# Performance work log

Hardware: AMD Instinct MI355X
Metric: run time of the kernel (lower is better)

Reference implementation:

```python
import jax, jax.numpy as jnp
import numpy as np

D_MODEL = 1024
D_FF = 4096
NUM_EXPERTS = 8
TOP_K = 2  # expert_capacity


def setup_inputs() -> dict:
    key = jax.random.key(0)
    ks = jax.random.split(key, 7)
    s_in = 1.0 / np.sqrt(D_MODEL)
    s_ff = 1.0 / np.sqrt(D_FF)
    x = jax.random.normal(ks[0], (2, 2048, D_MODEL), dtype=jnp.float32)
    gate_w = jax.random.uniform(ks[1], (NUM_EXPERTS, D_MODEL), jnp.float32, -s_in, s_in)
    gate_b = jax.random.uniform(ks[2], (NUM_EXPERTS,), jnp.float32, -s_in, s_in)
    w1 = jax.random.uniform(ks[3], (NUM_EXPERTS, D_MODEL, D_FF), jnp.float32, -s_in, s_in)
    b1 = jax.random.uniform(ks[4], (NUM_EXPERTS, D_FF), jnp.float32, -s_in, s_in)
    w2 = jax.random.uniform(ks[5], (NUM_EXPERTS, D_FF, D_MODEL), jnp.float32, -s_ff, s_ff)
    b2 = jax.random.uniform(ks[6], (NUM_EXPERTS, D_MODEL), jnp.float32, -s_ff, s_ff)
    return {"x": x, "gate_w": gate_w, "gate_b": gate_b,
            "w1": w1, "b1": b1, "w2": w2, "b2": b2}


def reference(x, gate_w, gate_b, w1, b1, w2, b2):
    E = gate_w.shape[0]
    # Router
    logits = jnp.einsum('bsd,ed->bse', x, gate_w) + gate_b  # [B,S,E]
    top_vals, top_idx = jax.lax.top_k(logits, TOP_K)        # [B,S,K]
    top_w = jax.nn.softmax(top_vals, axis=-1)               # softmax over the top-k logits
    probs = jax.nn.softmax(logits, axis=-1)
    usage = probs.mean(axis=(0, 1))                         # [E]
    load_balancing_loss = E * jnp.sum(usage ** 2) - 1.0
    # Combine weights: sum over top-k slots of weight * one_hot(expert)
    combine = jnp.sum(top_w[..., None] * jax.nn.one_hot(top_idx, E, dtype=x.dtype), axis=2)  # [B,S,E]
    # All experts over all tokens (faithful to the naive dense-then-mask module)
    h = jax.nn.gelu(jnp.einsum('bsd,edf->ebsf', x, w1) + b1[:, None, None, :], approximate=False)
    expert_out = jnp.einsum('ebsf,efd->ebsd', h, w2) + b2[:, None, None, :]  # [E,B,S,D]
    output = jnp.einsum('bse,ebsd->bsd', combine, expert_out)
    return output, load_balancing_loss
```

## Files before the change

kernel.cpp:

```cpp
#include <hip/hip_runtime.h>
#include <hip/hip_bf16.h>
#include <math.h>


#define D_MODEL 1024
#define D_FF    4096
#define NE      8
#define NTOK    4096
#define CAP     4096

typedef __attribute__((ext_vector_type(4))) float f32x4;
typedef __attribute__((ext_vector_type(8))) short s16x8;

__device__ __forceinline__ short f2bf(float f) {
    union { float f; unsigned u; } v; v.f = f;
    unsigned r = v.u + 0x7FFFu + ((v.u >> 16) & 1u);
    return (short)(r >> 16);
}

__device__ __forceinline__ void gload16(const void* g, void* l) {
    __builtin_amdgcn_global_load_lds(
        (const __attribute__((address_space(1))) unsigned*)g,
        (__attribute__((address_space(3))) unsigned*)l, 16, 0, 0);
}

__global__ __launch_bounds__(256) void router_kernel(
    const float* __restrict__ x, const float* __restrict__ gw,
    const float* __restrict__ gb,
    float* __restrict__ usage, int* __restrict__ eidx, float* __restrict__ wgt)
{
    __shared__ float s_gw[NE][D_MODEL];
    __shared__ float s_usage[NE];
    int tid = threadIdx.x;
    for (int i = tid * 4; i < NE * D_MODEL; i += 256 * 4)
        *(f32x4*)&s_gw[0][i] = *(const f32x4*)(gw + i);
    if (tid < NE) s_usage[tid] = 0.f;
    __syncthreads();

    int wid = tid >> 6, lane = tid & 63;
    int wave_stride = gridDim.x * 4;
    float l_usage[NE];
#pragma unroll
    for (int e = 0; e < NE; e++) l_usage[e] = 0.f;

    for (int t = blockIdx.x * 4 + wid; t < NTOK; t += wave_stride) {
        const float* xr = x + (size_t)t * D_MODEL;
        float acc[NE];
#pragma unroll
        for (int e = 0; e < NE; e++) acc[e] = 0.f;
        for (int i = lane * 4; i < D_MODEL; i += 64 * 4) {
            f32x4 xv = *(const f32x4*)(xr + i);
#pragma unroll
            for (int e = 0; e < NE; e++) {
                f32x4 gv = *(const f32x4*)&s_gw[e][i];
                acc[e] += xv[0]*gv[0] + xv[1]*gv[1] + xv[2]*gv[2] + xv[3]*gv[3];
            }
        }
#pragma unroll
        for (int e = 0; e < NE; e++) {
            float a = acc[e];
            for (int off = 32; off; off >>= 1) a += __shfl_down(a, off);
            acc[e] = a;
        }
        if (lane == 0) {
            float logits[NE];
            float mx = -1e30f;
#pragma unroll
            for (int e = 0; e < NE; e++) { logits[e] = acc[e] + gb[e]; mx = fmaxf(mx, logits[e]); }
            float se = 0.f;
            float pe[NE];
#pragma unroll
            for (int e = 0; e < NE; e++) { pe[e] = expf(logits[e] - mx); se += pe[e]; }
            float inv = 1.f / se;
#pragma unroll
            for (int e = 0; e < NE; e++) l_usage[e] += pe[e] * inv;
            int i0 = 0;
#pragma unroll
            for (int e = 1; e < NE; e++) if (logits[e] > logits[i0]) i0 = e;
            int i1 = -1;
#pragma unroll
            for (int e = 0; e < NE; e++) {
                if (e == i0) continue;
                if (i1 < 0 || logits[e] > logits[i1]) i1 = e;
            }
            float w0 = 1.f / (1.f + expf(logits[i1] - logits[i0]));
            eidx[t] = i0 | (i1 << 8);
            wgt[t] = w0;
        }
    }
    if (lane == 0) {
#pragma unroll
        for (int e = 0; e < NE; e++) atomicAdd(&s_usage[e], l_usage[e]);
    }
    __syncthreads();
    if (tid < NE) atomicAdd(&usage[tid], s_usage[tid]);
}

__global__ __launch_bounds__(256) void build_lists(
    const int* __restrict__ eidx, const float* __restrict__ wgt,
    int* __restrict__ cnt, int* __restrict__ tok_list, float* __restrict__ wt_list)
{
    int e = blockIdx.x;
    __shared__ int s_cnt;
    if (threadIdx.x == 0) s_cnt = 0;
    __syncthreads();
    for (int t = threadIdx.x; t < NTOK; t += 256) {
        int p = eidx[t];
        float w0 = wgt[t];
        if ((p & 255) == e) {
            int s = atomicAdd(&s_cnt, 1);
            tok_list[e * CAP + s] = t; wt_list[e * CAP + s] = w0;
        }
        if ((p >> 8) == e) {
            int s = atomicAdd(&s_cnt, 1);
            tok_list[e * CAP + s] = t; wt_list[e * CAP + s] = 1.f - w0;
        }
    }
    __syncthreads();
    if (threadIdx.x == 0) cnt[e] = s_cnt;
}

__global__ void compute_offsets(const int* __restrict__ cnt, int* __restrict__ offsets)
{
    int o = 0;
    for (int e = 0; e < NE; e++) { offsets[e] = o; o += cnt[e]; }
}

__global__ void write_loss(const float* __restrict__ usage, float* __restrict__ out_loss)
{
    float s = 0.f;
    for (int e = 0; e < NE; e++) { float u = usage[e] / (float)NTOK; s += u * u; }
    *out_loss = (float)NE * s - 1.f;
}

__global__ __launch_bounds__(256) void cvt_x_kernel(
    const float* __restrict__ x, short* __restrict__ xb)
{
    int i = (blockIdx.x * 256 + threadIdx.x) * 8;
    f32x4 a = *(const f32x4*)(x + i);
    f32x4 b = *(const f32x4*)(x + i + 4);
    s16x8 r;
    r[0]=f2bf(a[0]); r[1]=f2bf(a[1]); r[2]=f2bf(a[2]); r[3]=f2bf(a[3]);
    r[4]=f2bf(b[0]); r[5]=f2bf(b[1]); r[6]=f2bf(b[2]); r[7]=f2bf(b[3]);
    *(s16x8*)(xb + i) = r;
}

__global__ __launch_bounds__(256) void transpose_cvt(
    const float* __restrict__ src, short* __restrict__ dst, int R, int C)
{
    __shared__ float tile[64][65];
    int e = blockIdx.z;
    src += (size_t)e * R * C;
    dst += (size_t)e * R * C;
    int c0 = blockIdx.x * 64, r0 = blockIdx.y * 64;
    int tid = threadIdx.x;
    int lr = tid >> 2, lc = (tid & 3) * 16;

    const float* s = src + (size_t)(r0 + lr) * C + c0 + lc;
#pragma unroll
    for (int j = 0; j < 4; j++)
        *(f32x4*)&tile[lr][lc + j * 4] = *(const f32x4*)(s + j * 4);
    __syncthreads();

    short* d = dst + (size_t)(c0 + lr) * R + r0 + lc;
    s16x8 v0, v1;
#pragma unroll
    for (int j = 0; j < 8; j++) v0[j] = f2bf(tile[lc + j][lr]);
#pragma unroll
    for (int j = 0; j < 8; j++) v1[j] = f2bf(tile[lc + 8 + j][lr]);
    *(s16x8*)d = v0;
    *(s16x8*)(d + 8) = v1;
}

#define GEMM_STAGE(AS, BS, BUF, KT)                          \
    gload16(asrc0 + (KT), &AS[BUF][wid * 16][0]);            \
    gload16(asrc1 + (KT), &AS[BUF][64 + wid * 16][0]);       \
    gload16(bsrc0 + (KT), &BS[BUF][wid * 16][0]);            \
    gload16(bsrc1 + (KT), &BS[BUF][64 + wid * 16][0]);

#define GEMM_COMPUTE(AS, BS, BUF)                                              \
    {                                                                          \
        s16x8 a[4], b[4];                                                      \
        int cidx = (kgr ^ ((lrow >> 1) & 3)) * 8;                              \
        _Pragma("unroll")                                                      \
        for (int i = 0; i < 4; i++) {                                          \
            a[i] = *(const s16x8*)&AS[BUF][wr * 64 + i * 16 + lrow][cidx];     \
            b[i] = *(const s16x8*)&BS[BUF][wc * 64 + i * 16 + lrow][cidx];     \
        }                                                                      \
        _Pragma("unroll")                                                      \
        for (int i = 0; i < 4; i++)                                            \
            _Pragma("unroll")                                                  \
            for (int j = 0; j < 4; j++)                                        \
                acc[i][j] = __builtin_amdgcn_mfma_f32_16x16x32_bf16(           \
                    a[i], b[j], acc[i][j], 0, 0, 0);                           \
    }

__global__ __launch_bounds__(256) void gemm1_kernel(
    const short* __restrict__ XB, const short* __restrict__ W1T,
    const float* __restrict__ b1, const int* __restrict__ cnt,
    const int* __restrict__ offsets, const int* __restrict__ tok_list,
    short* __restrict__ H)
{
    int e  = blockIdx.y >> 5;
    int tm = blockIdx.y & 31;
    int ce = cnt[e];
    if (tm * 128 >= ce) return;
    int n0 = blockIdx.x * 128;

    __shared__ __align__(16) short As[2][128][32];
    __shared__ __align__(16) short Bs[2][128][32];

    int tid = threadIdx.x;
    int lane = tid & 63, wid = tid >> 6;
    int wr = wid >> 1, wc = wid & 1;
    int lrow = lane & 15, kgr = lane >> 4;

    int srow = wid * 16 + (lane >> 2);
    int scol = ((lane & 3) ^ ((lane >> 3) & 3)) * 8;
    int am0 = tm * 128 + srow, am1 = am0 + 64;
    int tok0 = tok_list[e * CAP + (am0 < ce ? am0 : 0)];
    int tok1 = tok_list[e * CAP + (am1 < ce ? am1 : 0)];
    const short* asrc0 = XB + (size_t)tok0 * D_MODEL + scol;
    const short* asrc1 = XB + (size_t)tok1 * D_MODEL + scol;
    const short* bsrc0 = W1T + ((size_t)e * D_FF + n0 + srow) * D_MODEL + scol;
    const short* bsrc1 = bsrc0 + (size_t)64 * D_MODEL;

    f32x4 acc[4][4] = {};
    GEMM_STAGE(As, Bs, 0, 0);
    int cur = 0;
    for (int kt = 32; kt < D_MODEL; kt += 32) {
        GEMM_STAGE(As, Bs, cur ^ 1, kt);
        asm volatile("s_waitcnt vmcnt(4)" ::: "memory");
        __builtin_amdgcn_s_barrier();
        GEMM_COMPUTE(As, Bs, cur);
        __builtin_amdgcn_s_barrier();
        cur ^= 1;
    }
    asm volatile("s_waitcnt vmcnt(0)" ::: "memory");
    __builtin_amdgcn_s_barrier();
    GEMM_COMPUTE(As, Bs, cur);

    int offe = offsets[e];
    float bn[4];
#pragma unroll
    for (int j = 0; j < 4; j++) bn[j] = b1[e * D_FF + n0 + wc * 64 + j * 16 + lrow];
#pragma unroll
    for (int i = 0; i < 4; i++) {
#pragma unroll
        for (int q = 0; q < 4; q++) {
            int m = tm * 128 + wr * 64 + i * 16 + kgr * 4 + q;
            if (m >= ce) continue;
            short* hrow = H + (size_t)(offe + m) * D_FF;
#pragma unroll
            for (int j = 0; j < 4; j++) {
                int n = n0 + wc * 64 + j * 16 + lrow;
                float v = acc[i][j][q] + bn[j];
                v = 0.5f * v * (1.f + erff(v * 0.70710678118654752f));
                hrow[n] = f2bf(v);
            }
        }
    }
}

__global__ __launch_bounds__(256) void gemm2_kernel(
    const short* __restrict__ H, const short* __restrict__ W2T,
    const float* __restrict__ b2, const int* __restrict__ cnt,
    const int* __restrict__ offsets, const int* __restrict__ tok_list,
    const float* __restrict__ wt_list, float* __restrict__ out)
{
    int e  = blockIdx.y >> 5;
    int tm = blockIdx.y & 31;
    int ce = cnt[e];
    if (tm * 128 >= ce) return;
    int offe = offsets[e];
    int n0 = blockIdx.x * 128;
    int kz = blockIdx.z;
    const int KSPAN = D_FF / 2;
    int kbase = kz * KSPAN;

    __shared__ __align__(16) short As[2][128][32];
    __shared__ __align__(16) short Bs[2][128][32];

    int tid = threadIdx.x;
    int lane = tid & 63, wid = tid >> 6;
    int wr = wid >> 1, wc = wid & 1;
    int lrow = lane & 15, kgr = lane >> 4;

    int srow = wid * 16 + (lane >> 2);
    int scol = ((lane & 3) ^ ((lane >> 3) & 3)) * 8;
    int am0 = tm * 128 + srow, am1 = am0 + 64;
    const short* asrc0 = H + (size_t)(offe + (am0 < ce ? am0 : 0)) * D_FF + kbase + scol;
    const short* asrc1 = H + (size_t)(offe + (am1 < ce ? am1 : 0)) * D_FF + kbase + scol;
    const short* bsrc0 = W2T + ((size_t)e * D_MODEL + n0 + srow) * D_FF + kbase + scol;
    const short* bsrc1 = bsrc0 + (size_t)64 * D_FF;

    f32x4 acc[4][4] = {};
    GEMM_STAGE(As, Bs, 0, 0);
    int cur = 0;
    for (int kt = 32; kt < KSPAN; kt += 32) {
        GEMM_STAGE(As, Bs, cur ^ 1, kt);
        asm volatile("s_waitcnt vmcnt(4)" ::: "memory");
        __builtin_amdgcn_s_barrier();
        GEMM_COMPUTE(As, Bs, cur);
        __builtin_amdgcn_s_barrier();
        cur ^= 1;
    }
    asm volatile("s_waitcnt vmcnt(0)" ::: "memory");
    __builtin_amdgcn_s_barrier();
    GEMM_COMPUTE(As, Bs, cur);

    float bn[4];
#pragma unroll
    for (int j = 0; j < 4; j++)
        bn[j] = (kz == 0) ? b2[e * D_MODEL + n0 + wc * 64 + j * 16 + lrow] : 0.f;
#pragma unroll
    for (int i = 0; i < 4; i++) {
#pragma unroll
        for (int q = 0; q < 4; q++) {
            int m = tm * 128 + wr * 64 + i * 16 + kgr * 4 + q;
            if (m >= ce) continue;
            int tokm = tok_list[e * CAP + m];
            float wt = wt_list[e * CAP + m];
            float* orow = out + (size_t)tokm * D_MODEL;
#pragma unroll
            for (int j = 0; j < 4; j++) {
                int n = n0 + wc * 64 + j * 16 + lrow;
                atomicAdd(&orow[n], wt * (acc[i][j][q] + bn[j]));
            }
        }
    }
}

extern "C" void kernel_launch(void* const* d_in, const int* in_sizes, int n_in,
                              void* d_out, int out_size, void* d_ws, size_t ws_size,
                              hipStream_t stream)
{
    const float* x  = (const float*)d_in[0];
    const float* gw = (const float*)d_in[1];
    const float* gb = (const float*)d_in[2];
    const float* w1 = (const float*)d_in[3];
    const float* b1 = (const float*)d_in[4];
    const float* w2 = (const float*)d_in[5];
    const float* b2 = (const float*)d_in[6];
    float* out = (float*)d_out;

    char* w = (char*)d_ws;
    int*   cnt      = (int*)(w + 0);
    float* usage    = (float*)(w + 32);
    int*   offsets  = (int*)(w + 64);
    int*   tok_list = (int*)(w + 128);
    float* wt_list  = (float*)(w + 128 + NE * CAP * 4);
    short* WT       = (short*)(w + 128 + 2 * NE * CAP * 4);
    short* H        = (short*)((char*)WT + (size_t)NE * D_FF * D_MODEL * 2);
    int*   eidx     = (int*)WT;
    float* wgt      = (float*)(WT + NTOK * 2);
    short* XB       = (short*)d_out;

    hipMemsetAsync(d_ws, 0, 128, stream);

    router_kernel<<<256, 256, 0, stream>>>(x, gw, gb, usage, eidx, wgt);
    build_lists<<<NE, 256, 0, stream>>>(eidx, wgt, cnt, tok_list, wt_list);
    compute_offsets<<<1, 1, 0, stream>>>(cnt, offsets);
    cvt_x_kernel<<<NTOK * D_MODEL / (256 * 8), 256, 0, stream>>>(x, XB);

    transpose_cvt<<<dim3(D_FF / 64, D_MODEL / 64, NE), 256, 0, stream>>>(w1, WT, D_MODEL, D_FF);
    gemm1_kernel<<<dim3(D_FF / 128, NE * (CAP / 128)), 256, 0, stream>>>(
        XB, WT, b1, cnt, offsets, tok_list, H);

    hipMemsetAsync(d_out, 0, (size_t)out_size * sizeof(float), stream);
    write_loss<<<1, 1, 0, stream>>>(usage, out + (size_t)NTOK * D_MODEL);

    transpose_cvt<<<dim3(D_MODEL / 64, D_FF / 64, NE), 256, 0, stream>>>(w2, WT, D_FF, D_MODEL);
    gemm2_kernel<<<dim3(D_MODEL / 128, NE * (CAP / 128), 2), 256, 0, stream>>>(
        H, WT, b2, cnt, offsets, tok_list, wt_list, out);
}
```

Baseline: 389.9 us.

## Drop LDS double buffering in expert GEMMs and use tanh-approximate GELU

Both expert GEMM kernels stop double-buffering their LDS tiles. Each k-step now loads into a single buffer, syncs, computes and syncs again. This halves LDS use, which may let more blocks reside per CU, but it serialises global loads with MFMA work inside each block. Separately, the exact erf GELU is replaced by a tanh-style approximation built from exp and a fast reciprocal, which cuts epilogue cost but changes numerics slightly from the exact GELU the reference specifies.

```diff
diff --git a/kernel.cpp b/kernel.cpp
--- a/kernel.cpp
+++ b/kernel.cpp
@@ -16,6 +16,14 @@
     union { float f; unsigned u; } v; v.f = f;
     unsigned r = v.u + 0x7FFFu + ((v.u >> 16) & 1u);
     return (short)(r >> 16);
+}
+
+__device__ __forceinline__ float gelu_f(float x) {
+    float u = x * x;
+    float v = __builtin_fmaf(0.044715f, u, 1.0f);
+    float y2 = 1.5957691216057308f * x * v;
+    float r = __builtin_amdgcn_rcpf(__expf(y2) + 1.0f);
+    return x - x * r;
 }
 
 __device__ __forceinline__ void gload16(const void* g, void* l) {
@@ -172,20 +180,20 @@
     *(s16x8*)(d + 8) = v1;
 }
 
-#define GEMM_STAGE(AS, BS, BUF, KT)                          \
-    gload16(asrc0 + (KT), &AS[BUF][wid * 16][0]);            \
-    gload16(asrc1 + (KT), &AS[BUF][64 + wid * 16][0]);       \
-    gload16(bsrc0 + (KT), &BS[BUF][wid * 16][0]);            \
-    gload16(bsrc1 + (KT), &BS[BUF][64 + wid * 16][0]);
-
-#define GEMM_COMPUTE(AS, BS, BUF)                                              \
+#define GEMM_STAGE(AS, BS, KT)                       \
+    gload16(asrc0 + (KT), &AS[wid * 16][0]);         \
+    gload16(asrc1 + (KT), &AS[64 + wid * 16][0]);    \
+    gload16(bsrc0 + (KT), &BS[wid * 16][0]);         \
+    gload16(bsrc1 + (KT), &BS[64 + wid * 16][0]);
+
+#define GEMM_COMPUTE(AS, BS)                                                   \
     {                                                                          \
         s16x8 a[4], b[4];                                                      \
         int cidx = (kgr ^ ((lrow >> 1) & 3)) * 8;                              \
         _Pragma("unroll")                                                      \
         for (int i = 0; i < 4; i++) {                                          \
-            a[i] = *(const s16x8*)&AS[BUF][wr * 64 + i * 16 + lrow][cidx];     \
-            b[i] = *(const s16x8*)&BS[BUF][wc * 64 + i * 16 + lrow][cidx];     \
+            a[i] = *(const s16x8*)&AS[wr * 64 + i * 16 + lrow][cidx];          \
+            b[i] = *(const s16x8*)&BS[wc * 64 + i * 16 + lrow][cidx];          \
         }                                                                      \
         _Pragma("unroll")                                                      \
         for (int i = 0; i < 4; i++)                                            \
@@ -207,8 +215,8 @@
     if (tm * 128 >= ce) return;
     int n0 = blockIdx.x * 128;
 
-    __shared__ __align__(16) short As[2][128][32];
-    __shared__ __align__(16) short Bs[2][128][32];
+    __shared__ __align__(16) short As[128][32];
+    __shared__ __align__(16) short Bs[128][32];
 
     int tid = threadIdx.x;
     int lane = tid & 63, wid = tid >> 6;
@@ -226,19 +234,12 @@
     const short* bsrc1 = bsrc0 + (size_t)64 * D_MODEL;
 
     f32x4 acc[4][4] = {};
-    GEMM_STAGE(As, Bs, 0, 0);
-    int cur = 0;
-    for (int kt = 32; kt < D_MODEL; kt += 32) {
-        GEMM_STAGE(As, Bs, cur ^ 1, kt);
-        asm volatile("s_waitcnt vmcnt(4)" ::: "memory");
-        __builtin_amdgcn_s_barrier();
-        GEMM_COMPUTE(As, Bs, cur);
-        __builtin_amdgcn_s_barrier();
-        cur ^= 1;
-    }
-    asm volatile("s_waitcnt vmcnt(0)" ::: "memory");
-    __builtin_amdgcn_s_barrier();
-    GEMM_COMPUTE(As, Bs, cur);
+    for (int kt = 0; kt < D_MODEL; kt += 32) {
+        GEMM_STAGE(As, Bs, kt);
+        __syncthreads();
+        GEMM_COMPUTE(As, Bs);
+        __syncthreads();
+    }
 
     int offe = offsets[e];
     float bn[4];
@@ -254,9 +255,7 @@
 #pragma unroll
             for (int j = 0; j < 4; j++) {
                 int n = n0 + wc * 64 + j * 16 + lrow;
-                float v = acc[i][j][q] + bn[j];
-                v = 0.5f * v * (1.f + erff(v * 0.70710678118654752f));
-                hrow[n] = f2bf(v);
+                hrow[n] = f2bf(gelu_f(acc[i][j][q] + bn[j]));
             }
         }
     }
@@ -278,8 +277,8 @@
     const int KSPAN = D_FF / 2;
     int kbase = kz * KSPAN;
 
-    __shared__ __align__(16) short As[2][128][32];
-    __shared__ __align__(16) short Bs[2][128][32];
+    __shared__ __align__(16) short As[128][32];
+    __shared__ __align__(16) short Bs[128][32];
 
     int tid = threadIdx.x;
     int lane = tid & 63, wid = tid >> 6;
@@ -295,19 +294,12 @@
     const short* bsrc1 = bsrc0 + (size_t)64 * D_FF;
 
     f32x4 acc[4][4] = {};
-    GEMM_STAGE(As, Bs, 0, 0);
-    int cur = 0;
-    for (int kt = 32; kt < KSPAN; kt += 32) {
-        GEMM_STAGE(As, Bs, cur ^ 1, kt);
-        asm volatile("s_waitcnt vmcnt(4)" ::: "memory");
-        __builtin_amdgcn_s_barrier();
-        GEMM_COMPUTE(As, Bs, cur);
-        __builtin_amdgcn_s_barrier();
-        cur ^= 1;
-    }
-    asm volatile("s_waitcnt vmcnt(0)" ::: "memory");
-    __builtin_amdgcn_s_barrier();
-    GEMM_COMPUTE(As, Bs, cur);
+    for (int kt = 0; kt < KSPAN; kt += 32) {
+        GEMM_STAGE(As, Bs, kt);
+        __syncthreads();
+        GEMM_COMPUTE(As, Bs);
+        __syncthreads();
+    }
 
     float bn[4];
 #pragma unroll
```

Result: faster. 365.0 us (-6.4%).
